# Kernel tuning notes

Measured on AMD Instinct MI355X. Metric: run time of the kernel, lower is better.

## Reference

```python
import jax, jax.numpy as jnp
import numpy as np


def pfaffian(A):
    """Pfaffian of even-dim skew-symmetric A via Parlett-Reid LTL^T (no pivoting).
    pf(A) = prod over elimination steps of the (k, k+1) pivot."""
    n = A.shape[0]
    ar = jnp.arange(n)

    def step(carry, i):
        A, pf = carry
        k = 2 * i
        pivot = A[k, k + 1]
        mask = ar > (k + 1)                      # rows/cols k+2:
        tau = jnp.where(mask, A[k, :], 0.0) / pivot
        col = jnp.where(mask, A[:, k + 1], 0.0)
        # rank-2 skew update of the trailing submatrix
        A = A + tau[:, None] * col[None, :] - col[:, None] * tau[None, :]
        return (A, pf * pivot), None

    (A, pf), _ = jax.lax.scan(step, (A, jnp.ones((), A.dtype)), jnp.arange(n // 2))
    return pf


def setup_inputs() -> dict:
    key = jax.random.key(0)
    k1, k2 = jax.random.split(key)
    N = 128          # nsites; Nparticle = N (spin system, one particle per site)
    B = 128          # batch of Monte-Carlo configurations
    x = jax.random.normal(k1, (B, N), jnp.float32)
    scale = np.float32(np.sqrt(np.e / N))
    F = jax.random.normal(k2, (N * (2 * N - 1),), jnp.float32) * scale
    return {"x": x, "F": F}


def reference(x, F):
    N = x.shape[-1]
    Nparticle = N
    twoN = 2 * N
    # scatter parameter vector into strict lower triangle, antisymmetrize
    F_full = jnp.zeros((twoN, twoN), F.dtype).at[jnp.tril_indices(twoN, -1)].set(F)
    F_full = F_full - F_full.T

    def single(xi):
        # spin system: up orbitals where x>0, down orbitals where x<=0
        occ = jnp.concatenate([xi > 0, xi <= 0])
        idx = jnp.flatnonzero(occ, size=Nparticle)
        A = F_full[idx[:, None], idx[None, :]]   # [Nparticle, Nparticle] gather
        return pfaffian(A)

    return jax.vmap(single)(x)
```

## Files before the change

### kernel.cpp

```cpp
#include <hip/hip_runtime.h>


#define POFF(i) ((i) + (((i) >> 5) << 2))
#define RL(v, l) __int_as_float(__builtin_amdgcn_readlane(__float_as_int(v), (l)))

__global__ __launch_bounds__(512) void pfaffian_kernel(
    const float* __restrict__ x,
    const float* __restrict__ F,
    float* __restrict__ out)
{
    const int b    = blockIdx.x;
    const int t    = threadIdx.x;
    const int lane = t & 63;
    const int wave = t >> 6;

    __shared__ int idx_sh[128];
    __shared__ int wtot[4];
    __shared__ __align__(16) float tauLDS[2][4][144];
    __shared__ __align__(16) float colLDS[2][4][144];
    __shared__ __align__(16) float rS[2][4][144];
    __shared__ __align__(16) float cS[2][4][144];

    if (t < 256) {
        const float xv  = x[b * 128 + (t & 127)];
        const bool  pos = xv > 0.0f;
        const bool  o   = (t < 128) ? pos : !pos;
        const unsigned long long mm = __ballot(o);
        const int rank = __popcll(mm & ((1ull << lane) - 1ull));
        if (lane == 63) wtot[wave] = rank + (o ? 1 : 0);
        __syncthreads();
        int off = 0;
#pragma unroll
        for (int w = 0; w < 4; ++w)
            if (w < wave) off += wtot[w];
        if (o) idx_sh[off + rank] = t;
    } else {
        __syncthreads();
    }
    __syncthreads();

    const int rg   = t >> 4;
    const int cg   = t & 15;
    const int row0 = rg << 2;
    const int col0 = cg << 3;
    const int prow = POFF(row0);
    const int pcol = POFF(col0);

    int ri[4], ci[8];
#pragma unroll
    for (int a = 0; a < 4; ++a) ri[a] = idx_sh[row0 + a];
#pragma unroll
    for (int c = 0; c < 8; ++c) ci[c] = idx_sh[col0 + c];

    float A[4][8];
#pragma unroll
    for (int a = 0; a < 4; ++a) {
        const int ii = ri[a];
#pragma unroll
        for (int c = 0; c < 8; ++c) {
            const int jj = ci[c];
            const int hi = ii > jj ? ii : jj;
            const int lo = ii > jj ? jj : ii;
            float v = (ii == jj) ? 0.0f : F[(hi * (hi - 1)) / 2 + lo];
            A[a][c] = (ii < jj) ? -v : v;
        }
    }

    auto stage = [&](int Pn, int st) {
        const int rgbase = 2 * Pn;
        if (rg == rgbase) {
            *(float4*)&rS[st][0][pcol]     = make_float4(A[0][0], A[0][1], A[0][2], A[0][3]);
            *(float4*)&rS[st][0][pcol + 4] = make_float4(A[0][4], A[0][5], A[0][6], A[0][7]);
            *(float4*)&rS[st][1][pcol]     = make_float4(A[2][0], A[2][1], A[2][2], A[2][3]);
            *(float4*)&rS[st][1][pcol + 4] = make_float4(A[2][4], A[2][5], A[2][6], A[2][7]);
        }
        if (rg == rgbase + 1) {
            *(float4*)&rS[st][2][pcol]     = make_float4(A[0][0], A[0][1], A[0][2], A[0][3]);
            *(float4*)&rS[st][2][pcol + 4] = make_float4(A[0][4], A[0][5], A[0][6], A[0][7]);
            *(float4*)&rS[st][3][pcol]     = make_float4(A[2][0], A[2][1], A[2][2], A[2][3]);
            *(float4*)&rS[st][3][pcol + 4] = make_float4(A[2][4], A[2][5], A[2][6], A[2][7]);
        }
        if (cg == Pn) {
            *(float4*)&cS[st][0][prow] = make_float4(A[0][1], A[1][1], A[2][1], A[3][1]);
            *(float4*)&cS[st][1][prow] = make_float4(A[0][3], A[1][3], A[2][3], A[3][3]);
            *(float4*)&cS[st][2][prow] = make_float4(A[0][5], A[1][5], A[2][5], A[3][5]);
            *(float4*)&cS[st][3][prow] = make_float4(A[0][7], A[1][7], A[2][7], A[3][7]);
        }
    };
    stage(0, 0);
    stage(1, 1);
    __syncthreads();

    float pf = 1.0f;
    float TAUp[4][2], CVp[4][2];

    auto crew = [&](int Pn, bool pre) {
        const int sv = Pn & 1;
        const int g0 = lane << 1;
        const int g1 = g0 + 1;
        const int pg = POFF(g0);
        float R[4][2], C[4][2];
#pragma unroll
        for (int j = 0; j < 4; ++j) {
            const float2 rv = *(const float2*)&rS[sv][j][pg];
            const float2 cv = *(const float2*)&cS[sv][j][pg];
            R[j][0] = rv.x; R[j][1] = rv.y;
            C[j][0] = cv.x; C[j][1] = cv.y;
        }
        if (pre) {
#pragma unroll
            for (int jp = 0; jp < 4; ++jp) {
#pragma unroll
                for (int a = 0; a < 4; ++a) {
                    const int la = 4 * Pn + a;
                    const float tau_r = RL(TAUp[jp][0], la);
                    const float col_r = RL(CVp[jp][0], la);
                    R[a][0] = __fmaf_rn(-col_r, TAUp[jp][0],
                              __fmaf_rn(tau_r, CVp[jp][0], R[a][0]));
                    R[a][1] = __fmaf_rn(-col_r, TAUp[jp][1],
                              __fmaf_rn(tau_r, CVp[jp][1], R[a][1]));
                    const float tau_c = RL(TAUp[jp][1], la);
                    const float col_c = RL(CVp[jp][1], la);
                    C[a][0] = __fmaf_rn(-CVp[jp][0], tau_c,
                              __fmaf_rn(TAUp[jp][0], col_c, C[a][0]));
                    C[a][1] = __fmaf_rn(-CVp[jp][1], tau_c,
                              __fmaf_rn(TAUp[jp][1], col_c, C[a][1]));
                }
            }
        }
        float TAU[4][2], CV[4][2];
#pragma unroll
        for (int j = 0; j < 4; ++j) {
            const int k = 8 * Pn + 2 * j;
            const float piv = RL(R[j][1], 4 * Pn + j);
            pf = __fmul_rn(pf, piv);
            TAU[j][0] = (g0 > k + 1) ? __fdiv_rn(R[j][0], piv) : 0.0f;
            TAU[j][1] = (g1 > k + 1) ? __fdiv_rn(R[j][1], piv) : 0.0f;
            CV[j][0]  = (g0 > k + 1) ? C[j][0] : 0.0f;
            CV[j][1]  = (g1 > k + 1) ? C[j][1] : 0.0f;
            *(float2*)&tauLDS[sv][j][pg] = make_float2(TAU[j][0], TAU[j][1]);
            *(float2*)&colLDS[sv][j][pg] = make_float2(CV[j][0], CV[j][1]);
#pragma unroll
            for (int j2 = j + 1; j2 < 4; ++j2) {
                const int ls = 4 * Pn + j2;
                const float tau_r = RL(TAU[j][0], ls);
                const float col_r = RL(CV[j][0], ls);
                R[j2][0] = __fmaf_rn(-col_r, TAU[j][0],
                           __fmaf_rn(tau_r, CV[j][0], R[j2][0]));
                R[j2][1] = __fmaf_rn(-col_r, TAU[j][1],
                           __fmaf_rn(tau_r, CV[j][1], R[j2][1]));
                const float tau_c = RL(TAU[j][1], ls);
                const float col_c = RL(CV[j][1], ls);
                C[j2][0] = __fmaf_rn(-CV[j][0], tau_c,
                           __fmaf_rn(TAU[j][0], col_c, C[j2][0]));
                C[j2][1] = __fmaf_rn(-CV[j][1], tau_c,
                           __fmaf_rn(TAU[j][1], col_c, C[j2][1]));
            }
        }
#pragma unroll
        for (int j = 0; j < 4; ++j) {
            TAUp[j][0] = TAU[j][0]; TAUp[j][1] = TAU[j][1];
            CVp[j][0]  = CV[j][0];  CVp[j][1]  = CV[j][1];
        }
    };

    if (wave == 0) crew(0, false);
    __syncthreads();

    for (int P = 0; P < 15; ++P) {
        if (wave >= 1 && 2 * wave > P) {
            const int sp = P & 1;
#pragma unroll
            for (int j = 0; j < 4; ++j) {
                const float4 trv = *(const float4*)&tauLDS[sp][j][prow];
                const float4 crv = *(const float4*)&colLDS[sp][j][prow];
                const float4 t0v = *(const float4*)&tauLDS[sp][j][pcol];
                const float4 t1v = *(const float4*)&tauLDS[sp][j][pcol + 4];
                const float4 c0v = *(const float4*)&colLDS[sp][j][pcol];
                const float4 c1v = *(const float4*)&colLDS[sp][j][pcol + 4];
                const float tr[4] = {trv.x, trv.y, trv.z, trv.w};
                const float cr[4] = {crv.x, crv.y, crv.z, crv.w};
                const float tc[8] = {t0v.x, t0v.y, t0v.z, t0v.w,
                                     t1v.x, t1v.y, t1v.z, t1v.w};
                const float cc[8] = {c0v.x, c0v.y, c0v.z, c0v.w,
                                     c1v.x, c1v.y, c1v.z, c1v.w};
#pragma unroll
                for (int a = 0; a < 4; ++a) {
#pragma unroll
                    for (int c = 0; c < 8; ++c) {
                        A[a][c] = __fmaf_rn(-cr[a], tc[c],
                                  __fmaf_rn(tr[a], cc[c], A[a][c]));
                    }
                }
            }
            if (P <= 13) stage(P + 2, P & 1);
        }
        if (wave == 0) crew(P + 1, true);
        __syncthreads();
    }

    if (t == 0) out[b] = pf;
}

extern "C" void kernel_launch(void* const* d_in, const int* in_sizes, int n_in,
                              void* d_out, int out_size, void* d_ws, size_t ws_size,
                              hipStream_t stream) {
    const float* x = (const float*)d_in[0];
    const float* F = (const float*)d_in[1];
    float* out     = (float*)d_out;
    (void)in_sizes; (void)n_in; (void)out_size; (void)d_ws; (void)ws_size;

    pfaffian_kernel<<<128, 512, 0, stream>>>(x, F, out);
}
```

Baseline: 76.18 us.

## Double panel width to eight pivots per step and read prior panel from LDS

Widens the blocked Parlett-Reid panel from four to eight elimination steps, halving the number of block-synchronised outer iterations from 15 to 7. Wave 0's look-ahead update of the next panel now reads the previous panel's tau/col vectors from LDS with vector loads instead of broadcasting them via readlane from registers. This cuts barrier count and readlane traffic but makes the serial panel factorisation in wave 0 longer, doubles the LDS buffers, and increases register pressure.

```diff
diff --git a/kernel.cpp b/kernel.cpp
--- a/kernel.cpp
+++ b/kernel.cpp
@@ -16,10 +16,10 @@
 
     __shared__ int idx_sh[128];
     __shared__ int wtot[4];
-    __shared__ __align__(16) float tauLDS[2][4][144];
-    __shared__ __align__(16) float colLDS[2][4][144];
-    __shared__ __align__(16) float rS[2][4][144];
-    __shared__ __align__(16) float cS[2][4][144];
+    __shared__ __align__(16) float tauLDS[2][8][144];
+    __shared__ __align__(16) float colLDS[2][8][144];
+    __shared__ __align__(16) float rS[2][8][144];
+    __shared__ __align__(16) float cS[2][8][144];
 
     if (t < 256) {
         const float xv  = x[b * 128 + (t & 127)];
@@ -67,72 +67,83 @@
     }
 
     auto stage = [&](int Pn, int st) {
-        const int rgbase = 2 * Pn;
-        if (rg == rgbase) {
-            *(float4*)&rS[st][0][pcol]     = make_float4(A[0][0], A[0][1], A[0][2], A[0][3]);
-            *(float4*)&rS[st][0][pcol + 4] = make_float4(A[0][4], A[0][5], A[0][6], A[0][7]);
-            *(float4*)&rS[st][1][pcol]     = make_float4(A[2][0], A[2][1], A[2][2], A[2][3]);
-            *(float4*)&rS[st][1][pcol + 4] = make_float4(A[2][4], A[2][5], A[2][6], A[2][7]);
-        }
-        if (rg == rgbase + 1) {
-            *(float4*)&rS[st][2][pcol]     = make_float4(A[0][0], A[0][1], A[0][2], A[0][3]);
-            *(float4*)&rS[st][2][pcol + 4] = make_float4(A[0][4], A[0][5], A[0][6], A[0][7]);
-            *(float4*)&rS[st][3][pcol]     = make_float4(A[2][0], A[2][1], A[2][2], A[2][3]);
-            *(float4*)&rS[st][3][pcol + 4] = make_float4(A[2][4], A[2][5], A[2][6], A[2][7]);
-        }
-        if (cg == Pn) {
-            *(float4*)&cS[st][0][prow] = make_float4(A[0][1], A[1][1], A[2][1], A[3][1]);
-            *(float4*)&cS[st][1][prow] = make_float4(A[0][3], A[1][3], A[2][3], A[3][3]);
-            *(float4*)&cS[st][2][prow] = make_float4(A[0][5], A[1][5], A[2][5], A[3][5]);
-            *(float4*)&cS[st][3][prow] = make_float4(A[0][7], A[1][7], A[2][7], A[3][7]);
+        const int d = rg - 4 * Pn;
+        if (d >= 0 && d < 4) {
+            *(float4*)&rS[st][2 * d][pcol]         = make_float4(A[0][0], A[0][1], A[0][2], A[0][3]);
+            *(float4*)&rS[st][2 * d][pcol + 4]     = make_float4(A[0][4], A[0][5], A[0][6], A[0][7]);
+            *(float4*)&rS[st][2 * d + 1][pcol]     = make_float4(A[2][0], A[2][1], A[2][2], A[2][3]);
+            *(float4*)&rS[st][2 * d + 1][pcol + 4] = make_float4(A[2][4], A[2][5], A[2][6], A[2][7]);
+        }
+        const int e = cg - 2 * Pn;
+        if (e == 0 || e == 1) {
+            const int mb = 4 * e;
+            *(float4*)&cS[st][mb][prow]     = make_float4(A[0][1], A[1][1], A[2][1], A[3][1]);
+            *(float4*)&cS[st][mb + 1][prow] = make_float4(A[0][3], A[1][3], A[2][3], A[3][3]);
+            *(float4*)&cS[st][mb + 2][prow] = make_float4(A[0][5], A[1][5], A[2][5], A[3][5]);
+            *(float4*)&cS[st][mb + 3][prow] = make_float4(A[0][7], A[1][7], A[2][7], A[3][7]);
         }
     };
     stage(0, 0);
     stage(1, 1);
-    __syncthreads();
 
     float pf = 1.0f;
-    float TAUp[4][2], CVp[4][2];
 
     auto crew = [&](int Pn, bool pre) {
         const int sv = Pn & 1;
         const int g0 = lane << 1;
         const int g1 = g0 + 1;
         const int pg = POFF(g0);
-        float R[4][2], C[4][2];
-#pragma unroll
-        for (int j = 0; j < 4; ++j) {
+        float R[8][2], C[8][2];
+#pragma unroll
+        for (int j = 0; j < 8; ++j) {
             const float2 rv = *(const float2*)&rS[sv][j][pg];
             const float2 cv = *(const float2*)&cS[sv][j][pg];
             R[j][0] = rv.x; R[j][1] = rv.y;
             C[j][0] = cv.x; C[j][1] = cv.y;
         }
         if (pre) {
-#pragma unroll
-            for (int jp = 0; jp < 4; ++jp) {
-#pragma unroll
-                for (int a = 0; a < 4; ++a) {
-                    const int la = 4 * Pn + a;
-                    const float tau_r = RL(TAUp[jp][0], la);
-                    const float col_r = RL(CVp[jp][0], la);
-                    R[a][0] = __fmaf_rn(-col_r, TAUp[jp][0],
-                              __fmaf_rn(tau_r, CVp[jp][0], R[a][0]));
-                    R[a][1] = __fmaf_rn(-col_r, TAUp[jp][1],
-                              __fmaf_rn(tau_r, CVp[jp][1], R[a][1]));
-                    const float tau_c = RL(TAUp[jp][1], la);
-                    const float col_c = RL(CVp[jp][1], la);
-                    C[a][0] = __fmaf_rn(-CVp[jp][0], tau_c,
-                              __fmaf_rn(TAUp[jp][0], col_c, C[a][0]));
-                    C[a][1] = __fmaf_rn(-CVp[jp][1], tau_c,
-                              __fmaf_rn(TAUp[jp][1], col_c, C[a][1]));
+            const int svp  = sv ^ 1;
+            const int base = POFF(16 * Pn);
+#pragma unroll
+            for (int jp = 0; jp < 8; ++jp) {
+                float4 Tq[4], Cq[4];
+#pragma unroll
+                for (int q = 0; q < 4; ++q) {
+                    Tq[q] = *(const float4*)&tauLDS[svp][jp][base + 4 * q];
+                    Cq[q] = *(const float4*)&colLDS[svp][jp][base + 4 * q];
+                }
+                const float trA[8] = {Tq[0].x, Tq[0].z, Tq[1].x, Tq[1].z,
+                                      Tq[2].x, Tq[2].z, Tq[3].x, Tq[3].z};
+                const float crA[8] = {Cq[0].x, Cq[0].z, Cq[1].x, Cq[1].z,
+                                      Cq[2].x, Cq[2].z, Cq[3].x, Cq[3].z};
+                const float tcA[8] = {Tq[0].y, Tq[0].w, Tq[1].y, Tq[1].w,
+                                      Tq[2].y, Tq[2].w, Tq[3].y, Tq[3].w};
+                const float ccA[8] = {Cq[0].y, Cq[0].w, Cq[1].y, Cq[1].w,
+                                      Cq[2].y, Cq[2].w, Cq[3].y, Cq[3].w};
+                const float2 tpv = *(const float2*)&tauLDS[svp][jp][pg];
+                const float2 cpv = *(const float2*)&colLDS[svp][jp][pg];
+#pragma unroll
+                for (int a = 0; a < 8; ++a) {
+                    const float tau_r = trA[a];
+                    const float col_r = crA[a];
+                    R[a][0] = __fmaf_rn(-col_r, tpv.x,
+                              __fmaf_rn(tau_r, cpv.x, R[a][0]));
+                    R[a][1] = __fmaf_rn(-col_r, tpv.y,
+                              __fmaf_rn(tau_r, cpv.y, R[a][1]));
+                    const float tau_c = tcA[a];
+                    const float col_c = ccA[a];
+                    C[a][0] = __fmaf_rn(-cpv.x, tau_c,
+                              __fmaf_rn(tpv.x, col_c, C[a][0]));
+                    C[a][1] = __fmaf_rn(-cpv.y, tau_c,
+                              __fmaf_rn(tpv.y, col_c, C[a][1]));
                 }
             }
         }
-        float TAU[4][2], CV[4][2];
-#pragma unroll
-        for (int j = 0; j < 4; ++j) {
-            const int k = 8 * Pn + 2 * j;
-            const float piv = RL(R[j][1], 4 * Pn + j);
+        float TAU[8][2], CV[8][2];
+#pragma unroll
+        for (int j = 0; j < 8; ++j) {
+            const int k = 16 * Pn + 2 * j;
+            const float piv = RL(R[j][1], 8 * Pn + j);
             pf = __fmul_rn(pf, piv);
             TAU[j][0] = (g0 > k + 1) ? __fdiv_rn(R[j][0], piv) : 0.0f;
             TAU[j][1] = (g1 > k + 1) ? __fdiv_rn(R[j][1], piv) : 0.0f;
@@ -141,8 +152,8 @@
             *(float2*)&tauLDS[sv][j][pg] = make_float2(TAU[j][0], TAU[j][1]);
             *(float2*)&colLDS[sv][j][pg] = make_float2(CV[j][0], CV[j][1]);
 #pragma unroll
-            for (int j2 = j + 1; j2 < 4; ++j2) {
-                const int ls = 4 * Pn + j2;
+            for (int j2 = j + 1; j2 < 8; ++j2) {
+                const int ls = 8 * Pn + j2;
                 const float tau_r = RL(TAU[j][0], ls);
                 const float col_r = RL(CV[j][0], ls);
                 R[j2][0] = __fmaf_rn(-col_r, TAU[j][0],
@@ -157,21 +168,17 @@
                            __fmaf_rn(TAU[j][1], col_c, C[j2][1]));
             }
         }
-#pragma unroll
-        for (int j = 0; j < 4; ++j) {
-            TAUp[j][0] = TAU[j][0]; TAUp[j][1] = TAU[j][1];
-            CVp[j][0]  = CV[j][0];  CVp[j][1]  = CV[j][1];
-        }
     };
 
+    __syncthreads();
     if (wave == 0) crew(0, false);
     __syncthreads();
 
-    for (int P = 0; P < 15; ++P) {
-        if (wave >= 1 && 2 * wave > P) {
+    for (int P = 0; P < 7; ++P) {
+        if (wave > P) {
             const int sp = P & 1;
 #pragma unroll
-            for (int j = 0; j < 4; ++j) {
+            for (int j = 0; j < 8; ++j) {
                 const float4 trv = *(const float4*)&tauLDS[sp][j][prow];
                 const float4 crv = *(const float4*)&colLDS[sp][j][prow];
                 const float4 t0v = *(const float4*)&tauLDS[sp][j][pcol];
@@ -193,7 +200,7 @@
                     }
                 }
             }
-            if (P <= 13) stage(P + 2, P & 1);
+            if (P <= 5) stage(P + 2, P & 1);
         }
         if (wave == 0) crew(P + 1, true);
         __syncthreads();
```

Result: slower. 78.13 us (+2.6%).
